# Kernel optimization log

Measured on AMD Instinct MI355X. Metric: run time of the kernel, lower is better.

## Reference

```python
import jax, jax.numpy as jnp
import numpy as np

N_NODES = 100000
N_EDGES = 1000000
IN_CH = 64
HID = 64
PROJ = 128
N_GRAPHS = 64
BN_EPS = 1e-5


def _glorot(key, shape):
    fan_in, fan_out = shape[0], shape[1]
    lim = (6.0 / (fan_in + fan_out)) ** 0.5
    return jax.random.uniform(key, shape, jnp.float32, -lim, lim)


def setup_inputs() -> dict:
    key = jax.random.key(0)
    ks = jax.random.split(key, 16)
    x = jax.random.normal(ks[0], (N_NODES, IN_CH), jnp.float32)
    edge_index = jax.random.randint(ks[1], (2, N_EDGES), 0, N_NODES, jnp.int64)
    batch = jnp.sort(jax.random.randint(ks[2], (N_NODES,), 0, N_GRAPHS, jnp.int64))
    inp = {
        "x": x, "edge_index": edge_index, "batch": batch,
        # conv1 MLP: Linear(2*in, hid), Linear(hid, hid)
        "c1_w1": _glorot(ks[3], (2 * IN_CH, HID)), "c1_b1": jnp.zeros((HID,), jnp.float32),
        "c1_w2": _glorot(ks[4], (HID, HID)), "c1_b2": jnp.zeros((HID,), jnp.float32),
        "bn1_g": jnp.ones((HID,), jnp.float32), "bn1_b": jnp.zeros((HID,), jnp.float32),
        # conv2 MLP: Linear(2*hid, hid), Linear(hid, hid)
        "c2_w1": _glorot(ks[5], (2 * HID, HID)), "c2_b1": jnp.zeros((HID,), jnp.float32),
        "c2_w2": _glorot(ks[6], (HID, HID)), "c2_b2": jnp.zeros((HID,), jnp.float32),
        "bn2_g": jnp.ones((HID,), jnp.float32), "bn2_b": jnp.zeros((HID,), jnp.float32),
        # projector: Linear(2*hid, proj), BN(proj), Linear(proj, proj)
        "p_w1": _glorot(ks[7], (2 * HID, PROJ)), "p_b1": jnp.zeros((PROJ,), jnp.float32),
        "p_bng": jnp.ones((PROJ,), jnp.float32), "p_bnb": jnp.zeros((PROJ,), jnp.float32),
        "p_w2": _glorot(ks[8], (PROJ, PROJ)), "p_b2": jnp.zeros((PROJ,), jnp.float32),
    }
    return inp


def _edge_conv(x, src, dst, w1, b1, w2, b2):
    # PyG EdgeConv: message = nn(cat([x_i, x_j - x_i])), aggr = max over incoming edges
    xi = x[dst]                                   # [E, C] target features
    xj = x[src]                                   # [E, C] source features
    m = jnp.concatenate([xi, xj - xi], axis=-1)   # [E, 2C]
    h = jax.nn.relu(m @ w1 + b1)
    h = jax.nn.relu(h @ w2 + b2)                  # [E, H]
    out = jax.ops.segment_max(h, dst, num_segments=N_NODES)
    return jnp.where(jnp.isfinite(out), out, 0.0)  # nodes w/o in-edges -> 0


def _batchnorm(x, g, b):
    mu = jnp.mean(x, axis=0)
    var = jnp.mean((x - mu) ** 2, axis=0)  # biased var (training-mode BN)
    return (x - mu) * jax.lax.rsqrt(var + BN_EPS) * g + b


def reference(x, edge_index, batch,
              c1_w1, c1_b1, c1_w2, c1_b2, bn1_g, bn1_b,
              c2_w1, c2_b1, c2_w2, c2_b2, bn2_g, bn2_b,
              p_w1, p_b1, p_bng, p_bnb, p_w2, p_b2):
    src, dst = edge_index[0], edge_index[1]
    h = _edge_conv(x, src, dst, c1_w1, c1_b1, c1_w2, c1_b2)
    h = _batchnorm(h, bn1_g, bn1_b)
    h = _edge_conv(h, src, dst, c2_w1, c2_b1, c2_w2, c2_b2)
    x_node = _batchnorm(h, bn2_g, bn2_b)            # [N, H]
    # graph pooling
    counts = jax.ops.segment_sum(jnp.ones((N_NODES,), x_node.dtype), batch,
                                 num_segments=N_GRAPHS)
    mean_pool = jax.ops.segment_sum(x_node, batch, num_segments=N_GRAPHS) / \
        jnp.maximum(counts, 1.0)[:, None]
    max_pool = jax.ops.segment_max(x_node, batch, num_segments=N_GRAPHS)
    max_pool = jnp.where(jnp.isfinite(max_pool), max_pool, 0.0)
    x_graph = jnp.concatenate([mean_pool, max_pool], axis=1)  # [G, 2H]
    # projector MLP
    z = x_graph @ p_w1 + p_b1
    z = jax.nn.relu(_batchnorm(z, p_bng, p_bnb))
    z_proj = z @ p_w2 + p_b2                        # [G, PROJ]
    return (z_proj, x_node, x_graph)
```

## Files before the change

### kernel.cpp

```cpp
#include <hip/hip_runtime.h>
#include <hip/hip_fp16.h>

constexpr int NN = 100000;
constexpr int NE = 1000000;
constexpr int NG = 64;
constexpr float BN_EPS = 1e-5f;
constexpr int NTILES = NE / 32;
constexpr int NNTILES = NN / 32;
constexpr int NREC = NTILES * 2;
constexpr int TPW = 4;

constexpr int NBUK = 196;
constexpr int BINB = 256;
constexpr int BCHUNK = (NE + BINB - 1) / BINB;
constexpr int TABN = NBUK * BINB;

constexpr long H1R_OFF  = 0;
constexpr long XNR_OFF  = 3200000;
constexpr long PART_OFF = 6400000;
constexpr long SC1_OFF  = PART_OFF + 32768;
constexpr long SH1_OFF  = SC1_OFF + 64;
constexpr long SC2_OFF  = SH1_OFF + 64;
constexpr long SH2_OFF  = SC2_OFF + 64;
constexpr long PSUM_OFF = SH2_OFF + 64;
constexpr long PMAX_OFF = PSUM_OFF + 4096;
constexpr long CNT_OFF  = PMAX_OFF + 4096;
constexpr long TICK_OFF = CNT_OFF + 64;
constexpr long TAB_OFF  = TICK_OFF + 16;
constexpr long SEDG_OFF = TAB_OFF + 50176;
constexpr long WF1_OFF  = SEDG_OFF + 2000000;
constexpr long WF2_OFF  = WF1_OFF + 6144;
constexpr long RECD_OFF = WF2_OFF + 6144;
constexpr long RECV_OFF = RECD_OFF + 62528;
constexpr long P_OFF    = RECV_OFF + 2000000;
constexpr long Q_OFF    = P_OFF + 3200000;

constexpr long OUT_XNODE = 8192;
constexpr long OUT_XG    = 8192 + 6400000L;

using f16x8 = __attribute__((ext_vector_type(8))) _Float16;
using f32x16 = __attribute__((ext_vector_type(16))) float;

__device__ __forceinline__ unsigned short f2h(float f) {
    return __builtin_bit_cast(unsigned short, (_Float16)f);
}
__device__ __forceinline__ unsigned pkrtz(float a, float b) {
    return __builtin_bit_cast(unsigned, __builtin_amdgcn_cvt_pkrtz(a, b));
}
__device__ __forceinline__ unsigned pk_add_f16(unsigned a, unsigned b) {
    unsigned d;
    asm("v_pk_add_f16 %0, %1, %2" : "=v"(d) : "v"(a), "v"(b));
    return d;
}
__device__ __forceinline__ unsigned pk_max_f16(unsigned a, unsigned b) {
    unsigned d;
    asm("v_pk_max_f16 %0, %1, %2" : "=v"(d) : "v"(a), "v"(b));
    return d;
}
__device__ __forceinline__ float h2f_lo(unsigned u) {
    return (float)__builtin_bit_cast(_Float16, (unsigned short)(u & 0xffffu));
}
__device__ __forceinline__ float h2f_hi(unsigned u) {
    return (float)__builtin_bit_cast(_Float16, (unsigned short)(u >> 16));
}
__device__ __forceinline__ unsigned fenc(float f) {
    unsigned u = __float_as_uint(f);
    return (u & 0x80000000u) ? ~u : (u | 0x80000000u);
}
__device__ __forceinline__ float fdec(unsigned u) {
    return (u & 0x80000000u) ? __uint_as_float(u & 0x7fffffffu) : __uint_as_float(~u);
}
__device__ __forceinline__ int xcd_swz(int bid, int nwg) {
    const int q = nwg >> 3, r = nwg & 7;
    const int x = bid & 7, i = bid >> 3;
    return (x < r ? x * (q + 1) : r * (q + 1) + (x - r) * q) + i;
}

__global__ __launch_bounds__(256) void bin_hist_kernel(
    const int* __restrict__ dst, int* __restrict__ tab)
{
    __shared__ int cnt[NBUK];
    const int t = threadIdx.x, b = blockIdx.x;
    if (t < NBUK) cnt[t] = 0;
    __syncthreads();
    const int lo = b * BCHUNK;
    const int hi = (lo + BCHUNK < NE) ? lo + BCHUNK : NE;
    for (int e = lo + t; e < hi; e += 256) atomicAdd(&cnt[dst[e] >> 9], 1);
    __syncthreads();
    if (t < NBUK) tab[t * BINB + b] = cnt[t];
}

__global__ __launch_bounds__(1024) void scan_tab_kernel(int* __restrict__ tab)
{
    __shared__ int part[1024];
    const int t = threadIdx.x;
    constexpr int VPT = 49;
    int vals[VPT];
    const int base = t * VPT;
    int s = 0;
    #pragma unroll
    for (int i = 0; i < VPT; ++i) {
        const int idx = base + i;
        const int v = (idx < TABN) ? tab[idx] : 0;
        vals[i] = v; s += v;
    }
    part[t] = s;
    __syncthreads();
    for (int off = 1; off < 1024; off <<= 1) {
        const int u = (t >= off) ? part[t - off] : 0;
        __syncthreads();
        part[t] += u;
        __syncthreads();
    }
    int run = (t == 0) ? 0 : part[t - 1];
    #pragma unroll
    for (int i = 0; i < VPT; ++i) {
        const int idx = base + i;
        if (idx < TABN) { const int v = vals[i]; tab[idx] = run; run += v; }
    }
}

__global__ __launch_bounds__(256) void bin_scatter_kernel(
    const int* __restrict__ src, const int* __restrict__ dst,
    const int* __restrict__ tab, int2* __restrict__ ebin)
{
    __shared__ int basec[NBUK];
    __shared__ int cur[NBUK];
    const int t = threadIdx.x, b = blockIdx.x;
    if (t < NBUK) { basec[t] = tab[t * BINB + b]; cur[t] = 0; }
    __syncthreads();
    const int lo = b * BCHUNK;
    const int hi = (lo + BCHUNK < NE) ? lo + BCHUNK : NE;
    for (int e = lo + t; e < hi; e += 256) {
        const int d = dst[e];
        const int k = d >> 9;
        const int pos = basec[k] + atomicAdd(&cur[k], 1);
        ebin[pos] = make_int2(src[e], d);
    }
}

__global__ __launch_bounds__(256) void bucket_sort_kernel(
    const int2* __restrict__ ebin, const int* __restrict__ tab,
    int2* __restrict__ sedge)
{
    __shared__ int hist[512];
    __shared__ int part[256];
    const int t = threadIdx.x, k = blockIdx.x;
    const int start = tab[k * BINB];
    const int end = (k == NBUK - 1) ? NE : tab[(k + 1) * BINB];
    hist[t * 2] = 0; hist[t * 2 + 1] = 0;
    __syncthreads();
    for (int e = start + t; e < end; e += 256) atomicAdd(&hist[ebin[e].y & 511], 1);
    __syncthreads();
    const int v0 = hist[t * 2], v1 = hist[t * 2 + 1];
    part[t] = v0 + v1;
    __syncthreads();
    for (int off = 1; off < 256; off <<= 1) {
        const int u = (t >= off) ? part[t - off] : 0;
        __syncthreads();
        part[t] += u;
        __syncthreads();
    }
    int run = (t == 0) ? 0 : part[t - 1];
    hist[t * 2] = run;
    hist[t * 2 + 1] = run + v0;
    __syncthreads();
    for (int e = start + t; e < end; e += 256) {
        const int2 v = ebin[e];
        const int pos = start + atomicAdd(&hist[v.y & 511], 1);
        sedge[pos] = v;
    }
}

__global__ __launch_bounds__(256) void prep_weights(
    const float* __restrict__ c1w1, const float* __restrict__ c1w2,
    const float* __restrict__ c2w1, const float* __restrict__ c2w2,
    unsigned short* __restrict__ wf)
{
    const int gidx = blockIdx.x * 256 + threadIdx.x;
    if (gidx >= 24576) return;
    const bool second = gidx >= 12288;
    const int idx = second ? gidx - 12288 : gidx;
    const float* __restrict__ w1 = second ? c2w1 : c1w1;
    const float* __restrict__ w2 = second ? c2w2 : c1w2;
    const int sec = idx >> 12;
    const int j = idx & 4095;
    const int f = j >> 9, rem = j & 511, ln = rem >> 3, i = rem & 7;
    const int t = f >> 2, ks = f & 3;
    const int k = ks * 16 + (ln >> 5) * 8 + i, c = t * 32 + (ln & 31);
    float v;
    if (sec == 0)      v = w1[k * 64 + c] - w1[(64 + k) * 64 + c];
    else if (sec == 1) v = w1[(64 + k) * 64 + c];
    else               v = w2[k * 64 + c];
    wf[gidx] = f2h(v);
}

template<bool NORM>
__global__ __launch_bounds__(256) void nodegemm_kernel(
    const void* __restrict__ xin,
    const unsigned short* __restrict__ wfrag,
    const float* __restrict__ b1,
    const float* __restrict__ scale, const float* __restrict__ shift,
    unsigned short* __restrict__ P, unsigned short* __restrict__ Q)
{
    __shared__ unsigned short wlds[8192];
    {
        const uint4* wsrc = reinterpret_cast<const uint4*>(wfrag);
        uint4* wdst = reinterpret_cast<uint4*>(wlds);
        #pragma unroll
        for (int i = 0; i < 4; ++i) wdst[threadIdx.x + i * 256] = wsrc[threadIdx.x + i * 256];
    }
    __syncthreads();

    const int wid = threadIdx.x >> 6, lane = threadIdx.x & 63;
    const int hi = lane >> 5, ln32 = lane & 31;
    const int tile = blockIdx.x * 4 + wid;
    if (tile >= NNTILES) return;
    const int node = tile * 32 + ln32;

    f32x16 cpa, cpb, cqa, cqb;
    #pragma unroll
    for (int r = 0; r < 16; ++r) {
        const int row = (r & 3) + 8 * (r >> 2) + 4 * hi;
        cpa[r] = b1[row]; cpb[r] = b1[32 + row];
        cqa[r] = 0.f;     cqb[r] = 0.f;
    }

    #pragma unroll
    for (int ks = 0; ks < 4; ++ks) {
        const int off = ks * 16 + hi * 8;
        float4 a, b;
        if constexpr (!NORM) {
            const float* xr = reinterpret_cast<const float*>(xin) + (long)node * 64;
            a = *reinterpret_cast<const float4*>(xr + off);
            b = *reinterpret_cast<const float4*>(xr + off + 4);
        } else {
            const unsigned* xr = reinterpret_cast<const unsigned*>(xin) + (long)node * 32;
            const uint4 u = *reinterpret_cast<const uint4*>(xr + ks * 8 + hi * 4);
            a.x = h2f_lo(u.x); a.y = h2f_hi(u.x); a.z = h2f_lo(u.y); a.w = h2f_hi(u.y);
            b.x = h2f_lo(u.z); b.y = h2f_hi(u.z); b.z = h2f_lo(u.w); b.w = h2f_hi(u.w);
            const float4 s0 = *reinterpret_cast<const float4*>(scale + off);
            const float4 s1 = *reinterpret_cast<const float4*>(scale + off + 4);
            const float4 h0 = *reinterpret_cast<const float4*>(shift + off);
            const float4 h1 = *reinterpret_cast<const float4*>(shift + off + 4);
            a.x = fmaf(a.x, s0.x, h0.x); a.y = fmaf(a.y, s0.y, h0.y);
            a.z = fmaf(a.z, s0.z, h0.z); a.w = fmaf(a.w, s0.w, h0.w);
            b.x = fmaf(b.x, s1.x, h1.x); b.y = fmaf(b.y, s1.y, h1.y);
            b.z = fmaf(b.z, s1.z, h1.z); b.w = fmaf(b.w, s1.w, h1.w);
        }
        uint4 uu;
        uu.x = pkrtz(a.x, a.y); uu.y = pkrtz(a.z, a.w);
        uu.z = pkrtz(b.x, b.y); uu.w = pkrtz(b.z, b.w);
        const f16x8 bfr = __builtin_bit_cast(f16x8, uu);
        const f16x8 ap0 = *reinterpret_cast<const f16x8*>(&wlds[(0 * 4 + ks) * 512 + lane * 8]);
        const f16x8 ap1 = *reinterpret_cast<const f16x8*>(&wlds[(1 * 4 + ks) * 512 + lane * 8]);
        const f16x8 aq0 = *reinterpret_cast<const f16x8*>(&wlds[4096 + (0 * 4 + ks) * 512 + lane * 8]);
        const f16x8 aq1 = *reinterpret_cast<const f16x8*>(&wlds[4096 + (1 * 4 + ks) * 512 + lane * 8]);
        cpa = __builtin_amdgcn_mfma_f32_32x32x16_f16(ap0, bfr, cpa, 0, 0, 0);
        cpb = __builtin_amdgcn_mfma_f32_32x32x16_f16(ap1, bfr, cpb, 0, 0, 0);
        cqa = __builtin_amdgcn_mfma_f32_32x32x16_f16(aq0, bfr, cqa, 0, 0, 0);
        cqb = __builtin_amdgcn_mfma_f32_32x32x16_f16(aq1, bfr, cqb, 0, 0, 0);
    }

    unsigned short* Pr = P + (long)node * 64;
    unsigned short* Qr = Q + (long)node * 64;
    #pragma unroll
    for (int t = 0; t < 2; ++t) {
        const f32x16 cp = t ? cpb : cpa;
        const f32x16 cq = t ? cqb : cqa;
        #pragma unroll
        for (int g2 = 0; g2 < 4; ++g2) {
            uint2 up, uq;
            up.x = pkrtz(cp[4 * g2 + 0], cp[4 * g2 + 1]);
            up.y = pkrtz(cp[4 * g2 + 2], cp[4 * g2 + 3]);
            uq.x = pkrtz(cq[4 * g2 + 0], cq[4 * g2 + 1]);
            uq.y = pkrtz(cq[4 * g2 + 2], cq[4 * g2 + 3]);
            const int co = t * 32 + 8 * g2 + 4 * hi;
            *reinterpret_cast<uint2*>(Pr + co) = up;
            *reinterpret_cast<uint2*>(Qr + co) = uq;
        }
    }
}

__global__ __launch_bounds__(256) void edgeconv_kernel(
    const unsigned short* __restrict__ P, const unsigned short* __restrict__ Q,
    const int2* __restrict__ sedge,
    const unsigned short* __restrict__ w2frag,
    const float* __restrict__ b2,
    unsigned* __restrict__ out,
    int* __restrict__ recd, unsigned* __restrict__ recv)
{
    __shared__ unsigned short wlds[4096];
    {
        const uint4* wsrc = reinterpret_cast<const uint4*>(w2frag);
        uint4* wdst = reinterpret_cast<uint4*>(wlds);
        #pragma unroll
        for (int i = 0; i < 2; ++i) wdst[threadIdx.x + i * 256] = wsrc[threadIdx.x + i * 256];
    }
    __syncthreads();

    const int wid  = threadIdx.x >> 6;
    const int lane = threadIdx.x & 63;
    const int hi   = lane >> 5;
    const int ln32 = lane & 31;
    const int tile0 = (xcd_swz(blockIdx.x, gridDim.x) * 4 + wid) * TPW;

    #pragma unroll 1
    for (int tt = 0; tt < TPW; ++tt) {
        const int tile = tile0 + tt;
        if (tile >= NTILES) break;

        const int2 sd = sedge[tile * 32 + ln32];
        const int s = sd.x, d = sd.y;
        const unsigned short* __restrict__ Pr = P + (long)d * 64;
        const unsigned short* __restrict__ Qr = Q + (long)s * 64;

        f32x16 c2a, c2b;
        #pragma unroll
        for (int r = 0; r < 16; ++r) {
            const int row = (r & 3) + 8 * (r >> 2) + 4 * hi;
            c2a[r] = b2[row];
            c2b[r] = b2[32 + row];
        }

        #pragma unroll
        for (int ks = 0; ks < 4; ++ks) {
            const int co = ks * 16 + hi * 8;
            const uint4 pu = *reinterpret_cast<const uint4*>(Pr + co);
            const uint4 qu = *reinterpret_cast<const uint4*>(Qr + co);
            uint4 hh;
            hh.x = pk_max_f16(pk_add_f16(pu.x, qu.x), 0u);
            hh.y = pk_max_f16(pk_add_f16(pu.y, qu.y), 0u);
            hh.z = pk_max_f16(pk_add_f16(pu.z, qu.z), 0u);
            hh.w = pk_max_f16(pk_add_f16(pu.w, qu.w), 0u);
            const f16x8 bfr = __builtin_bit_cast(f16x8, hh);
            const f16x8 a0 = *reinterpret_cast<const f16x8*>(&wlds[(0 * 4 + ks) * 512 + lane * 8]);
            const f16x8 a1 = *reinterpret_cast<const f16x8*>(&wlds[(1 * 4 + ks) * 512 + lane * 8]);
            c2a = __builtin_amdgcn_mfma_f32_32x32x16_f16(a0, bfr, c2a, 0, 0, 0);
            c2b = __builtin_amdgcn_mfma_f32_32x32x16_f16(a1, bfr, c2b, 0, 0, 0);
        }

        unsigned pkc[16];
        #pragma unroll
        for (int q = 0; q < 8; ++q) {
            pkc[q]     = pk_max_f16(pkrtz(c2a[2 * q], c2a[2 * q + 1]), 0u);
            pkc[8 + q] = pk_max_f16(pkrtz(c2b[2 * q], c2b[2 * q + 1]), 0u);
        }

        #pragma unroll
        for (int st = 1; st < 32; st <<= 1) {
            const int dn = __shfl_down(d, st, 32);
            const bool take = (ln32 + st < 32) && (dn == d);
            #pragma unroll
            for (int i = 0; i < 16; ++i) {
                const unsigned o = __shfl_down(pkc[i], st, 32);
                const unsigned m = pk_max_f16(pkc[i], o);
                pkc[i] = take ? m : pkc[i];
            }
        }
        const int dprev = __shfl_up(d, 1, 32);
        const bool leader = (ln32 == 0) || (d != dprev);
        const unsigned lm = (unsigned)(__ballot(leader) & 0xffffffffull);
        const int L31 = 31 - __builtin_clz(lm);

        if (leader) {
            if (ln32 != 0 && ln32 != L31) {
                unsigned* row = out + (long)d * 32;
                #pragma unroll
                for (int g2 = 0; g2 < 4; ++g2) {
                    *reinterpret_cast<uint2*>(row + 4 * g2 + 2 * hi) =
                        make_uint2(pkc[2 * g2], pkc[2 * g2 + 1]);
                    *reinterpret_cast<uint2*>(row + 16 + 4 * g2 + 2 * hi) =
                        make_uint2(pkc[8 + 2 * g2], pkc[8 + 2 * g2 + 1]);
                }
            }
            if (ln32 == 0) {
                unsigned* row = recv + (long)(tile * 2) * 32;
                #pragma unroll
                for (int g2 = 0; g2 < 4; ++g2) {
                    *reinterpret_cast<uint2*>(row + 4 * g2 + 2 * hi) =
                        make_uint2(pkc[2 * g2], pkc[2 * g2 + 1]);
                    *reinterpret_cast<uint2*>(row + 16 + 4 * g2 + 2 * hi) =
                        make_uint2(pkc[8 + 2 * g2], pkc[8 + 2 * g2 + 1]);
                }
                if (hi == 0) recd[tile * 2] = d;
            }
            if (ln32 == L31) {
                unsigned* row = recv + (long)(tile * 2 + 1) * 32;
                #pragma unroll
                for (int g2 = 0; g2 < 4; ++g2) {
                    *reinterpret_cast<uint2*>(row + 4 * g2 + 2 * hi) =
                        make_uint2(pkc[2 * g2], pkc[2 * g2 + 1]);
                    *reinterpret_cast<uint2*>(row + 16 + 4 * g2 + 2 * hi) =
                        make_uint2(pkc[8 + 2 * g2], pkc[8 + 2 * g2 + 1]);
                }
                if (hi == 0) recd[tile * 2 + 1] = d;
            }
        }
    }
}

__global__ __launch_bounds__(256) void fixup_kernel(
    const int* __restrict__ recd, const unsigned* __restrict__ recv,
    unsigned* __restrict__ out)
{
    const int wid = threadIdx.x >> 6;
    const int half = (threadIdx.x >> 5) & 1;
    const int c2 = threadIdx.x & 31;
    const int r = blockIdx.x * 8 + wid * 2 + half;
    if (r >= NREC) return;
    const int d = recd[r];
    int lo = r, hi = r;
    while (lo > 0 && recd[lo - 1] == d) --lo;
    while (hi + 1 < NREC && recd[hi + 1] == d) ++hi;
    unsigned m = 0u;
    for (int rr = lo; rr <= hi; ++rr) m = pk_max_f16(m, recv[(long)rr * 32 + c2]);
    out[(long)d * 32 + c2] = m;
}

__global__ __launch_bounds__(256) void stats_kernel(
    const unsigned* __restrict__ h, float* __restrict__ partial,
    const float* __restrict__ g, const float* __restrict__ b,
    float* __restrict__ scale, float* __restrict__ shift, int* __restrict__ ticket)
{
    __shared__ float red[4][256];
    __shared__ float red2[2][256];
    __shared__ int flag;
    const int tid = threadIdx.x;
    const int c2 = tid & 31, r = tid >> 5;
    float s0 = 0.f, ss0 = 0.f, s1 = 0.f, ss1 = 0.f;
    for (int v = blockIdx.x * 8 + r; v < NN; v += 256 * 8) {
        const unsigned u = h[(long)v * 32 + c2];
        const float a = h2f_lo(u), bb = h2f_hi(u);
        s0 += a; ss0 += a * a; s1 += bb; ss1 += bb * bb;
    }
    red[0][tid] = s0; red[1][tid] = ss0; red[2][tid] = s1; red[3][tid] = ss1;
    __syncthreads();
    if (r == 0) {
        float S0 = 0.f, SS0 = 0.f, S1 = 0.f, SS1 = 0.f;
        #pragma unroll
        for (int q = 0; q < 8; ++q) {
            S0 += red[0][c2 + q * 32]; SS0 += red[1][c2 + q * 32];
            S1 += red[2][c2 + q * 32]; SS1 += red[3][c2 + q * 32];
        }
        partial[blockIdx.x * 128 + 2 * c2]     = S0;
        partial[blockIdx.x * 128 + 2 * c2 + 1] = S1;
        partial[blockIdx.x * 128 + 64 + 2 * c2]     = SS0;
        partial[blockIdx.x * 128 + 64 + 2 * c2 + 1] = SS1;
    }
    __syncthreads();
    if (tid == 0) {
        __threadfence();
        flag = (atomicAdd(ticket, 1) == 255) ? 1 : 0;
    }
    __syncthreads();
    if (!flag) return;
    __threadfence();
    const int c = tid & 63, q = tid >> 6;
    float S = 0.f, SS = 0.f;
    for (int bb2 = q * 64; bb2 < q * 64 + 64; ++bb2) {
        S += partial[bb2 * 128 + c];
        SS += partial[bb2 * 128 + 64 + c];
    }
    red2[0][tid] = S; red2[1][tid] = SS;
    __syncthreads();
    if (q == 0) {
        #pragma unroll
        for (int p = 1; p < 4; ++p) { S += red2[0][c + p * 64]; SS += red2[1][c + p * 64]; }
        const float invN = 1.0f / (float)NN;
        const float mu = S * invN;
        const float var = SS * invN - mu * mu;
        const float sc = g[c] * rsqrtf(var + BN_EPS);
        scale[c] = sc;
        shift[c] = b[c] - mu * sc;
    }
}

constexpr int NPB = 256;
__global__ __launch_bounds__(256) void nodepass_kernel(
    const unsigned* __restrict__ xnr, float* __restrict__ xn,
    const int* __restrict__ batch,
    const float* __restrict__ scale, const float* __restrict__ shift,
    float* __restrict__ poolsum, unsigned* __restrict__ poolmax, int* __restrict__ counts)
{
    const int base = blockIdx.x * NPB;
    const int r = threadIdx.x >> 5, c2 = threadIdx.x & 31;
    const float sc0 = scale[2 * c2], sc1 = scale[2 * c2 + 1];
    const float sh0 = shift[2 * c2], sh1 = shift[2 * c2 + 1];
    int curg = -1; float rs0 = 0.f, rs1 = 0.f, rm0 = -INFINITY, rm1 = -INFINITY; int rc = 0;
    const int vend = (base + NPB < NN) ? base + NPB : NN;
    for (int v = base + r; v < vend; v += 8) {
        const unsigned u = xnr[(long)v * 32 + c2];
        const float v0 = fmaf(h2f_lo(u), sc0, sh0);
        const float v1 = fmaf(h2f_hi(u), sc1, sh1);
        *reinterpret_cast<float2*>(xn + (long)v * 64 + 2 * c2) = make_float2(v0, v1);
        const int g = batch[v];
        if (g != curg) {
            if (curg >= 0) {
                atomicAdd(poolsum + curg * 64 + 2 * c2, rs0);
                atomicAdd(poolsum + curg * 64 + 2 * c2 + 1, rs1);
                atomicMax(poolmax + curg * 64 + 2 * c2, fenc(rm0));
                atomicMax(poolmax + curg * 64 + 2 * c2 + 1, fenc(rm1));
                if (c2 == 0) atomicAdd(counts + curg, rc);
            }
            curg = g; rs0 = rs1 = 0.f; rm0 = rm1 = -INFINITY; rc = 0;
        }
        rs0 += v0; rs1 += v1; rm0 = fmaxf(rm0, v0); rm1 = fmaxf(rm1, v1); ++rc;
    }
    if (curg >= 0) {
        atomicAdd(poolsum + curg * 64 + 2 * c2, rs0);
        atomicAdd(poolsum + curg * 64 + 2 * c2 + 1, rs1);
        atomicMax(poolmax + curg * 64 + 2 * c2, fenc(rm0));
        atomicMax(poolmax + curg * 64 + 2 * c2 + 1, fenc(rm1));
        if (c2 == 0) atomicAdd(counts + curg, rc);
    }
}

__global__ __launch_bounds__(1024) void final_kernel(
    const float* __restrict__ poolsum, const unsigned* __restrict__ poolmax,
    const int* __restrict__ counts,
    const float* __restrict__ p_w1, const float* __restrict__ p_b1,
    const float* __restrict__ p_bng, const float* __restrict__ p_bnb,
    const float* __restrict__ p_w2, const float* __restrict__ p_b2,
    float* __restrict__ out)
{
    __shared__ float xg[64][128];
    __shared__ float znl[64 * 129];
    __shared__ float red[2][1024];
    __shared__ float scsh[2][128];
    const int tid = threadIdx.x;

    #pragma unroll
    for (int i = 0; i < 8; ++i) {
        const int e2 = tid + i * 1024;
        const int g = e2 >> 7, col = e2 & 127;
        float val;
        if (col < 64) {
            const float cnt = fmaxf((float)counts[g], 1.f);
            val = poolsum[g * 64 + col] / cnt;
        } else {
            const unsigned u = poolmax[g * 64 + col - 64];
            val = (u == 0u) ? 0.f : fdec(u);
        }
        xg[g][col] = val;
        out[OUT_XG + e2] = val;
    }
    __syncthreads();

    const int gg = tid >> 7, t = tid & 127;
    float z[8];
    #pragma unroll
    for (int gi = 0; gi < 8; ++gi) z[gi] = p_b1[t];
    for (int j = 0; j < 128; ++j) {
        const float wv = p_w1[j * 128 + t];
        #pragma unroll
        for (int gi = 0; gi < 8; ++gi) z[gi] = fmaf(xg[gg * 8 + gi][j], wv, z[gi]);
    }

    float s = 0.f, ss = 0.f;
    #pragma unroll
    for (int gi = 0; gi < 8; ++gi) { s += z[gi]; ss += z[gi] * z[gi]; }
    red[0][tid] = s; red[1][tid] = ss;
    __syncthreads();
    if (gg == 0) {
        float S = 0.f, SS = 0.f;
        #pragma unroll
        for (int q = 0; q < 8; ++q) { S += red[0][t + q * 128]; SS += red[1][t + q * 128]; }
        const float mu = S / 64.f;
        const float var = SS / 64.f - mu * mu;
        const float sc = p_bng[t] * rsqrtf(var + BN_EPS);
        scsh[0][t] = sc;
        scsh[1][t] = p_bnb[t] - mu * sc;
    }
    __syncthreads();
    const float sc = scsh[0][t], sh = scsh[1][t];
    #pragma unroll
    for (int gi = 0; gi < 8; ++gi) {
        const float zn = fmaxf(fmaf(z[gi], sc, sh), 0.f);
        znl[(gg * 8 + gi) * 129 + t] = zn;
    }
    __syncthreads();

    float zp[8];
    #pragma unroll
    for (int gi = 0; gi < 8; ++gi) zp[gi] = p_b2[t];
    for (int c = 0; c < 128; ++c) {
        const float wv = p_w2[c * 128 + t];
        #pragma unroll
        for (int gi = 0; gi < 8; ++gi) zp[gi] = fmaf(znl[(gg * 8 + gi) * 129 + c], wv, zp[gi]);
    }
    #pragma unroll
    for (int gi = 0; gi < 8; ++gi) out[(gg * 8 + gi) * 128 + t] = zp[gi];
}

extern "C" void kernel_launch(void* const* d_in, const int* in_sizes, int n_in,
                              void* d_out, int out_size, void* d_ws, size_t ws_size,
                              hipStream_t stream)
{
    const float* x     = (const float*)d_in[0];
    const int*   eidx  = (const int*)d_in[1];
    const int*   batch = (const int*)d_in[2];
    const float* c1w1  = (const float*)d_in[3];
    const float* c1b1  = (const float*)d_in[4];
    const float* c1w2  = (const float*)d_in[5];
    const float* c1b2  = (const float*)d_in[6];
    const float* bn1g  = (const float*)d_in[7];
    const float* bn1b  = (const float*)d_in[8];
    const float* c2w1  = (const float*)d_in[9];
    const float* c2b1  = (const float*)d_in[10];
    const float* c2w2  = (const float*)d_in[11];
    const float* c2b2  = (const float*)d_in[12];
    const float* bn2g  = (const float*)d_in[13];
    const float* bn2b  = (const float*)d_in[14];
    const float* pw1   = (const float*)d_in[15];
    const float* pb1   = (const float*)d_in[16];
    const float* pbng  = (const float*)d_in[17];
    const float* pbnb  = (const float*)d_in[18];
    const float* pw2   = (const float*)d_in[19];
    const float* pb2   = (const float*)d_in[20];

    const int* src = eidx;
    const int* dst = eidx + NE;

    float* ws  = (float*)d_ws;
    float* o   = (float*)d_out;
    unsigned* h1r = (unsigned*)(ws + H1R_OFF);
    unsigned* xnr = (unsigned*)(ws + XNR_OFF);
    float* xnode = o + OUT_XNODE;
    int* tick  = (int*)(ws + TICK_OFF);
    int* tab   = (int*)(ws + TAB_OFF);
    int2* ebin  = (int2*)(ws + H1R_OFF);
    int2* sedge = (int2*)(ws + SEDG_OFF);
    unsigned short* wf1 = (unsigned short*)(ws + WF1_OFF);
    unsigned short* wf2 = (unsigned short*)(ws + WF2_OFF);
    int* recd  = (int*)(ws + RECD_OFF);
    unsigned* recv = (unsigned*)(ws + RECV_OFF);
    unsigned short* Pb = (unsigned short*)(ws + P_OFF);
    unsigned short* Qb = (unsigned short*)(ws + Q_OFF);

    hipMemsetAsync(ws + PSUM_OFF, 0, (4096 + 4096 + 64 + 16) * 4, stream);

    prep_weights<<<96, 256, 0, stream>>>(c1w1, c1w2, c2w1, c2w2, wf1);

    bin_hist_kernel<<<BINB, 256, 0, stream>>>(dst, tab);
    scan_tab_kernel<<<1, 1024, 0, stream>>>(tab);
    bin_scatter_kernel<<<BINB, 256, 0, stream>>>(src, dst, tab, ebin);
    bucket_sort_kernel<<<NBUK, 256, 0, stream>>>(ebin, tab, sedge);

    hipMemsetAsync(h1r, 0, (size_t)NN * 64 * 2 * 2, stream);

    const int ngGrid   = (NNTILES + 3) / 4;
    const int convGrid = (NTILES + 4 * TPW - 1) / (4 * TPW);
    const int fixGrid  = (NREC + 7) / 8;

    nodegemm_kernel<false><<<ngGrid, 256, 0, stream>>>(
        x, wf1, c1b1, nullptr, nullptr, Pb, Qb);
    edgeconv_kernel<<<convGrid, 256, 0, stream>>>(
        Pb, Qb, sedge, wf1 + 8192, c1b2, h1r, recd, recv);
    fixup_kernel<<<fixGrid, 256, 0, stream>>>(recd, recv, h1r);
    stats_kernel<<<256, 256, 0, stream>>>(h1r, ws + PART_OFF, bn1g, bn1b,
                                          ws + SC1_OFF, ws + SH1_OFF, tick + 1);
    nodegemm_kernel<true><<<ngGrid, 256, 0, stream>>>(
        h1r, wf2, c2b1, ws + SC1_OFF, ws + SH1_OFF, Pb, Qb);
    edgeconv_kernel<<<convGrid, 256, 0, stream>>>(
        Pb, Qb, sedge, wf2 + 8192, c2b2, xnr, recd, recv);
    fixup_kernel<<<fixGrid, 256, 0, stream>>>(recd, recv, xnr);
    stats_kernel<<<256, 256, 0, stream>>>(xnr, ws + PART_OFF, bn2g, bn2b,
                                          ws + SC2_OFF, ws + SH2_OFF, tick + 2);
    nodepass_kernel<<<(NN + NPB - 1) / NPB, 256, 0, stream>>>(
        xnr, xnode, batch, ws + SC2_OFF, ws + SH2_OFF,
        ws + PSUM_OFF, (unsigned*)(ws + PMAX_OFF), (int*)(ws + CNT_OFF));
    final_kernel<<<1, 1024, 0, stream>>>(
        ws + PSUM_OFF, (unsigned*)(ws + PMAX_OFF), (int*)(ws + CNT_OFF),
        pw1, pb1, pbng, pbnb, pw2, pb2, o);
}
```

Before: 368.4 us.

## Replace memsets with targeted zeroing and give each edgeconv wave one tile

The full memset of the h1r/xnr buffers is replaced by zeroing only the rows of nodes with no in-edges inside bucket_sort_kernel, and the pool accumulator memset is folded into prep_weights. To make this possible, ebin moves from the h1r region into the recv region. edgeconv now processes one tile per wave instead of four, with a larger grid and an occupancy hint in launch_bounds. The aim is to cut memset traffic and launch count and to raise memory-level parallelism in edgeconv, at the cost of more blocks and a repeated LDS weight load per block.

```diff
diff --git a/kernel.cpp b/kernel.cpp
--- a/kernel.cpp
+++ b/kernel.cpp
@@ -8,7 +8,6 @@
 constexpr int NTILES = NE / 32;
 constexpr int NNTILES = NN / 32;
 constexpr int NREC = NTILES * 2;
-constexpr int TPW = 4;
 
 constexpr int NBUK = 196;
 constexpr int BINB = 256;
@@ -34,6 +33,7 @@
 constexpr long RECV_OFF = RECD_OFF + 62528;
 constexpr long P_OFF    = RECV_OFF + 2000000;
 constexpr long Q_OFF    = P_OFF + 3200000;
+constexpr int  POOLW    = 4096 + 4096 + 64 + 16;
 
 constexpr long OUT_XNODE = 8192;
 constexpr long OUT_XG    = 8192 + 6400000L;
@@ -141,7 +141,8 @@
 
 __global__ __launch_bounds__(256) void bucket_sort_kernel(
     const int2* __restrict__ ebin, const int* __restrict__ tab,
-    int2* __restrict__ sedge)
+    int2* __restrict__ sedge,
+    unsigned* __restrict__ h1r, unsigned* __restrict__ xnr)
 {
     __shared__ int hist[512];
     __shared__ int part[256];
@@ -153,6 +154,20 @@
     for (int e = start + t; e < end; e += 256) atomicAdd(&hist[ebin[e].y & 511], 1);
     __syncthreads();
     const int v0 = hist[t * 2], v1 = hist[t * 2 + 1];
+    {
+        const uint4 z = make_uint4(0u, 0u, 0u, 0u);
+        #pragma unroll
+        for (int j = 0; j < 2; ++j) {
+            const int node = k * 512 + t * 2 + j;
+            const int c = j ? v1 : v0;
+            if (node < NN && c == 0) {
+                uint4* r0 = reinterpret_cast<uint4*>(h1r + (long)node * 32);
+                uint4* r1 = reinterpret_cast<uint4*>(xnr + (long)node * 32);
+                #pragma unroll
+                for (int q2 = 0; q2 < 8; ++q2) { r0[q2] = z; r1[q2] = z; }
+            }
+        }
+    }
     part[t] = v0 + v1;
     __syncthreads();
     for (int off = 1; off < 256; off <<= 1) {
@@ -175,10 +190,14 @@
 __global__ __launch_bounds__(256) void prep_weights(
     const float* __restrict__ c1w1, const float* __restrict__ c1w2,
     const float* __restrict__ c2w1, const float* __restrict__ c2w2,
-    unsigned short* __restrict__ wf)
+    unsigned short* __restrict__ wf, float* __restrict__ pools)
 {
     const int gidx = blockIdx.x * 256 + threadIdx.x;
-    if (gidx >= 24576) return;
+    if (gidx >= 24576) {
+        const int z = gidx - 24576;
+        if (z < POOLW) pools[z] = 0.f;
+        return;
+    }
     const bool second = gidx >= 12288;
     const int idx = second ? gidx - 12288 : gidx;
     const float* __restrict__ w1 = second ? c2w1 : c1w1;
@@ -282,7 +301,7 @@
     }
 }
 
-__global__ __launch_bounds__(256) void edgeconv_kernel(
+__global__ __launch_bounds__(256, 8) void edgeconv_kernel(
     const unsigned short* __restrict__ P, const unsigned short* __restrict__ Q,
     const int2* __restrict__ sedge,
     const unsigned short* __restrict__ w2frag,
@@ -303,99 +322,94 @@
     const int lane = threadIdx.x & 63;
     const int hi   = lane >> 5;
     const int ln32 = lane & 31;
-    const int tile0 = (xcd_swz(blockIdx.x, gridDim.x) * 4 + wid) * TPW;
-
-    #pragma unroll 1
-    for (int tt = 0; tt < TPW; ++tt) {
-        const int tile = tile0 + tt;
-        if (tile >= NTILES) break;
-
-        const int2 sd = sedge[tile * 32 + ln32];
-        const int s = sd.x, d = sd.y;
-        const unsigned short* __restrict__ Pr = P + (long)d * 64;
-        const unsigned short* __restrict__ Qr = Q + (long)s * 64;
-
-        f32x16 c2a, c2b;
-        #pragma unroll
-        for (int r = 0; r < 16; ++r) {
-            const int row = (r & 3) + 8 * (r >> 2) + 4 * hi;
-            c2a[r] = b2[row];
-            c2b[r] = b2[32 + row];
-        }
-
-        #pragma unroll
-        for (int ks = 0; ks < 4; ++ks) {
-            const int co = ks * 16 + hi * 8;
-            const uint4 pu = *reinterpret_cast<const uint4*>(Pr + co);
-            const uint4 qu = *reinterpret_cast<const uint4*>(Qr + co);
-            uint4 hh;
-            hh.x = pk_max_f16(pk_add_f16(pu.x, qu.x), 0u);
-            hh.y = pk_max_f16(pk_add_f16(pu.y, qu.y), 0u);
-            hh.z = pk_max_f16(pk_add_f16(pu.z, qu.z), 0u);
-            hh.w = pk_max_f16(pk_add_f16(pu.w, qu.w), 0u);
-            const f16x8 bfr = __builtin_bit_cast(f16x8, hh);
-            const f16x8 a0 = *reinterpret_cast<const f16x8*>(&wlds[(0 * 4 + ks) * 512 + lane * 8]);
-            const f16x8 a1 = *reinterpret_cast<const f16x8*>(&wlds[(1 * 4 + ks) * 512 + lane * 8]);
-            c2a = __builtin_amdgcn_mfma_f32_32x32x16_f16(a0, bfr, c2a, 0, 0, 0);
-            c2b = __builtin_amdgcn_mfma_f32_32x32x16_f16(a1, bfr, c2b, 0, 0, 0);
-        }
-
-        unsigned pkc[16];
-        #pragma unroll
-        for (int q = 0; q < 8; ++q) {
-            pkc[q]     = pk_max_f16(pkrtz(c2a[2 * q], c2a[2 * q + 1]), 0u);
-            pkc[8 + q] = pk_max_f16(pkrtz(c2b[2 * q], c2b[2 * q + 1]), 0u);
-        }
-
-        #pragma unroll
-        for (int st = 1; st < 32; st <<= 1) {
-            const int dn = __shfl_down(d, st, 32);
-            const bool take = (ln32 + st < 32) && (dn == d);
+    const int tile = xcd_swz(blockIdx.x, gridDim.x) * 4 + wid;
+    if (tile >= NTILES) return;
+
+    const int2 sd = sedge[tile * 32 + ln32];
+    const int s = sd.x, d = sd.y;
+    const unsigned short* __restrict__ Pr = P + (long)d * 64;
+    const unsigned short* __restrict__ Qr = Q + (long)s * 64;
+
+    f32x16 c2a, c2b;
+    #pragma unroll
+    for (int r = 0; r < 16; ++r) {
+        const int row = (r & 3) + 8 * (r >> 2) + 4 * hi;
+        c2a[r] = b2[row];
+        c2b[r] = b2[32 + row];
+    }
+
+    #pragma unroll
+    for (int ks = 0; ks < 4; ++ks) {
+        const int co = ks * 16 + hi * 8;
+        const uint4 pu = *reinterpret_cast<const uint4*>(Pr + co);
+        const uint4 qu = *reinterpret_cast<const uint4*>(Qr + co);
+        uint4 hh;
+        hh.x = pk_max_f16(pk_add_f16(pu.x, qu.x), 0u);
+        hh.y = pk_max_f16(pk_add_f16(pu.y, qu.y), 0u);
+        hh.z = pk_max_f16(pk_add_f16(pu.z, qu.z), 0u);
+        hh.w = pk_max_f16(pk_add_f16(pu.w, qu.w), 0u);
+        const f16x8 bfr = __builtin_bit_cast(f16x8, hh);
+        const f16x8 a0 = *reinterpret_cast<const f16x8*>(&wlds[(0 * 4 + ks) * 512 + lane * 8]);
+        const f16x8 a1 = *reinterpret_cast<const f16x8*>(&wlds[(1 * 4 + ks) * 512 + lane * 8]);
+        c2a = __builtin_amdgcn_mfma_f32_32x32x16_f16(a0, bfr, c2a, 0, 0, 0);
+        c2b = __builtin_amdgcn_mfma_f32_32x32x16_f16(a1, bfr, c2b, 0, 0, 0);
+    }
+
+    unsigned pkc[16];
+    #pragma unroll
+    for (int q = 0; q < 8; ++q) {
+        pkc[q]     = pk_max_f16(pkrtz(c2a[2 * q], c2a[2 * q + 1]), 0u);
+        pkc[8 + q] = pk_max_f16(pkrtz(c2b[2 * q], c2b[2 * q + 1]), 0u);
+    }
+
+    #pragma unroll
+    for (int st = 1; st < 32; st <<= 1) {
+        const int dn = __shfl_down(d, st, 32);
+        const bool take = (ln32 + st < 32) && (dn == d);
+        #pragma unroll
+        for (int i = 0; i < 16; ++i) {
+            const unsigned o = __shfl_down(pkc[i], st, 32);
+            const unsigned m = pk_max_f16(pkc[i], o);
+            pkc[i] = take ? m : pkc[i];
+        }
+    }
+    const int dprev = __shfl_up(d, 1, 32);
+    const bool leader = (ln32 == 0) || (d != dprev);
+    const unsigned lm = (unsigned)(__ballot(leader) & 0xffffffffull);
+    const int L31 = 31 - __builtin_clz(lm);
+
+    if (leader) {
+        if (ln32 != 0 && ln32 != L31) {
+            unsigned* row = out + (long)d * 32;
             #pragma unroll
-            for (int i = 0; i < 16; ++i) {
-                const unsigned o = __shfl_down(pkc[i], st, 32);
-                const unsigned m = pk_max_f16(pkc[i], o);
-                pkc[i] = take ? m : pkc[i];
+            for (int g2 = 0; g2 < 4; ++g2) {
+                *reinterpret_cast<uint2*>(row + 4 * g2 + 2 * hi) =
+                    make_uint2(pkc[2 * g2], pkc[2 * g2 + 1]);
+                *reinterpret_cast<uint2*>(row + 16 + 4 * g2 + 2 * hi) =
+                    make_uint2(pkc[8 + 2 * g2], pkc[8 + 2 * g2 + 1]);
             }
         }
-        const int dprev = __shfl_up(d, 1, 32);
-        const bool leader = (ln32 == 0) || (d != dprev);
-        const unsigned lm = (unsigned)(__ballot(leader) & 0xffffffffull);
-        const int L31 = 31 - __builtin_clz(lm);
-
-        if (leader) {
-            if (ln32 != 0 && ln32 != L31) {
-                unsigned* row = out + (long)d * 32;
-                #pragma unroll
-                for (int g2 = 0; g2 < 4; ++g2) {
-                    *reinterpret_cast<uint2*>(row + 4 * g2 + 2 * hi) =
-                        make_uint2(pkc[2 * g2], pkc[2 * g2 + 1]);
-                    *reinterpret_cast<uint2*>(row + 16 + 4 * g2 + 2 * hi) =
-                        make_uint2(pkc[8 + 2 * g2], pkc[8 + 2 * g2 + 1]);
-                }
+        if (ln32 == 0) {
+            unsigned* row = recv + (long)(tile * 2) * 32;
+            #pragma unroll
+            for (int g2 = 0; g2 < 4; ++g2) {
+                *reinterpret_cast<uint2*>(row + 4 * g2 + 2 * hi) =
+                    make_uint2(pkc[2 * g2], pkc[2 * g2 + 1]);
+                *reinterpret_cast<uint2*>(row + 16 + 4 * g2 + 2 * hi) =
+                    make_uint2(pkc[8 + 2 * g2], pkc[8 + 2 * g2 + 1]);
             }
-            if (ln32 == 0) {
-                unsigned* row = recv + (long)(tile * 2) * 32;
-                #pragma unroll
-                for (int g2 = 0; g2 < 4; ++g2) {
-                    *reinterpret_cast<uint2*>(row + 4 * g2 + 2 * hi) =
-                        make_uint2(pkc[2 * g2], pkc[2 * g2 + 1]);
-                    *reinterpret_cast<uint2*>(row + 16 + 4 * g2 + 2 * hi) =
-                        make_uint2(pkc[8 + 2 * g2], pkc[8 + 2 * g2 + 1]);
-                }
-                if (hi == 0) recd[tile * 2] = d;
+            if (hi == 0) recd[tile * 2] = d;
+        }
+        if (ln32 == L31) {
+            unsigned* row = recv + (long)(tile * 2 + 1) * 32;
+            #pragma unroll
+            for (int g2 = 0; g2 < 4; ++g2) {
+                *reinterpret_cast<uint2*>(row + 4 * g2 + 2 * hi) =
+                    make_uint2(pkc[2 * g2], pkc[2 * g2 + 1]);
+                *reinterpret_cast<uint2*>(row + 16 + 4 * g2 + 2 * hi) =
+                    make_uint2(pkc[8 + 2 * g2], pkc[8 + 2 * g2 + 1]);
             }
-            if (ln32 == L31) {
-                unsigned* row = recv + (long)(tile * 2 + 1) * 32;
-                #pragma unroll
-                for (int g2 = 0; g2 < 4; ++g2) {
-                    *reinterpret_cast<uint2*>(row + 4 * g2 + 2 * hi) =
-                        make_uint2(pkc[2 * g2], pkc[2 * g2 + 1]);
-                    *reinterpret_cast<uint2*>(row + 16 + 4 * g2 + 2 * hi) =
-                        make_uint2(pkc[8 + 2 * g2], pkc[8 + 2 * g2 + 1]);
-                }
-                if (hi == 0) recd[tile * 2 + 1] = d;
-            }
+            if (hi == 0) recd[tile * 2 + 1] = d;
         }
     }
 }
@@ -629,7 +643,7 @@
     float* xnode = o + OUT_XNODE;
     int* tick  = (int*)(ws + TICK_OFF);
     int* tab   = (int*)(ws + TAB_OFF);
-    int2* ebin  = (int2*)(ws + H1R_OFF);
+    int2* ebin  = (int2*)(ws + RECV_OFF);
     int2* sedge = (int2*)(ws + SEDG_OFF);
     unsigned short* wf1 = (unsigned short*)(ws + WF1_OFF);
     unsigned short* wf2 = (unsigned short*)(ws + WF2_OFF);
@@ -638,19 +652,15 @@
     unsigned short* Pb = (unsigned short*)(ws + P_OFF);
     unsigned short* Qb = (unsigned short*)(ws + Q_OFF);
 
-    hipMemsetAsync(ws + PSUM_OFF, 0, (4096 + 4096 + 64 + 16) * 4, stream);
-
-    prep_weights<<<96, 256, 0, stream>>>(c1w1, c1w2, c2w1, c2w2, wf1);
+    prep_weights<<<129, 256, 0, stream>>>(c1w1, c1w2, c2w1, c2w2, wf1, ws + PSUM_OFF);
 
     bin_hist_kernel<<<BINB, 256, 0, stream>>>(dst, tab);
     scan_tab_kernel<<<1, 1024, 0, stream>>>(tab);
     bin_scatter_kernel<<<BINB, 256, 0, stream>>>(src, dst, tab, ebin);
-    bucket_sort_kernel<<<NBUK, 256, 0, stream>>>(ebin, tab, sedge);
-
-    hipMemsetAsync(h1r, 0, (size_t)NN * 64 * 2 * 2, stream);
+    bucket_sort_kernel<<<NBUK, 256, 0, stream>>>(ebin, tab, sedge, h1r, xnr);
 
     const int ngGrid   = (NNTILES + 3) / 4;
-    const int convGrid = (NTILES + 4 * TPW - 1) / (4 * TPW);
+    const int convGrid = (NTILES + 3) / 4;
     const int fixGrid  = (NREC + 7) / 8;
 
     nodegemm_kernel<false><<<ngGrid, 256, 0, stream>>>(
```

Result: faster. 351.2 us (-4.7%).
